# Kernel tuning notes

Hardware: AMD Instinct MI355X
Metric: run time of the kernel (lower is better)

The kernel has to match this reference:

```python
import jax, jax.numpy as jnp
import numpy as np
from jax import lax

NUM_CLASSES = 21
MAX_OUT = 5          # max_output_size in tf.image.non_max_suppression
IOU_THR = 0.5        # NMS_IOU_THRESHOLD
CONF_THR = 0.5       # CONFIDENCE_THRESHOLD
NEG = -1e9           # stand-in for -inf score (suppressed / background)


def setup_inputs() -> dict:
    key = jax.random.key(0)
    k1, k2, k3 = jax.random.split(key, 3)
    B, N, C = 128, 8732, NUM_CLASSES
    logits = jax.random.normal(k1, (B, N, 4 + C), dtype=jnp.float32)
    # default boxes in corner format [ymin, xmin, ymax, xmax], valid geometry
    ctr = jax.random.uniform(k2, (N, 2), dtype=jnp.float32)                 # cy, cx
    sz = jax.random.uniform(k3, (N, 2), dtype=jnp.float32, minval=0.05, maxval=0.3)  # h, w
    default_boxes = jnp.clip(
        jnp.concatenate([ctr - sz / 2, ctr + sz / 2], axis=-1), 0.0, 1.0)
    return {"logits": logits, "default_boxes": default_boxes}


def _decode(loc, db):
    # db: [N,4] corners -> center/size (matches get_offset's tf.stack)
    cy = (db[:, 2] + db[:, 0]) / 2
    cx = (db[:, 3] + db[:, 1]) / 2
    h = db[:, 2] - db[:, 0]
    w = db[:, 3] - db[:, 1]
    # loc: [B,N,4] = (dy, dx, dh, dw)
    ncy = loc[..., 0] * h + cy
    ncx = loc[..., 1] * w + cx
    nh = jnp.exp(loc[..., 2]) * h
    nw = jnp.exp(loc[..., 3]) * w
    boxes = jnp.stack(
        [ncy - nh / 2, ncx - nw / 2, ncy + nh / 2, ncx + nw / 2], axis=-1)
    return jnp.clip(boxes, 0.0, 1.0)


def _iou_one_vs_all(box, boxes):
    # box [4], boxes [N,4], corner format
    tl = jnp.maximum(box[:2], boxes[:, :2])
    br = jnp.minimum(box[2:], boxes[:, 2:])
    wh = jnp.maximum(br - tl, 0.0)
    inter = wh[:, 0] * wh[:, 1]
    a1 = (box[2] - box[0]) * (box[3] - box[1])
    a2 = (boxes[:, 2] - boxes[:, 0]) * (boxes[:, 3] - boxes[:, 1])
    return inter / (a1 + a2 - inter + 1e-12)


def _nms_single(boxes, scores, classes_f):
    # boxes [N,4], scores [N] (background already set to NEG), classes_f [N] float
    def step(s, _):
        i = jnp.argmax(s)
        sc = s[i]
        b = boxes[i]
        valid = sc > CONF_THR  # score_threshold in tf NMS
        iou = _iou_one_vs_all(b, boxes)
        s = jnp.where(iou > IOU_THR, NEG, s)  # suppresses i too (IoU=1)
        return s, (b, classes_f[i], sc, valid)

    _, (bs, cs, ss, vs) = lax.scan(step, scores, None, length=MAX_OUT)
    # pad invalid slots with zeros (TF returns variable-length; we use fixed 5 + zero pad)
    bs = jnp.where(vs[:, None], bs, 0.0)
    cs = jnp.where(vs, cs, 0.0)
    ss = jnp.where(vs, ss, 0.0)
    return bs, cs[:, None], ss[:, None]  # [5,4], [5,1], [5,1]


def reference(logits, default_boxes):
    boxes = _decode(logits[..., :4], default_boxes)          # [B,N,4]
    probs = jax.nn.softmax(logits[..., 4:], axis=-1)         # [B,N,C]
    scores = jnp.max(probs, axis=-1)                          # [B,N]
    classes = jnp.argmax(probs, axis=-1)                      # [B,N] int
    # boolean_mask(classes != 0) expressed as score = -inf for background
    scores_eff = jnp.where(classes != 0, scores, NEG)
    det_b, det_c, det_s = jax.vmap(_nms_single)(
        boxes, scores_eff, classes.astype(jnp.float32))
    # pack detection_boxes / detection_classes / detection_scores -> [B,5,6]
    return jnp.concatenate([det_b, det_c, det_s], axis=-1)
```

## Files before the change

### kernel.cpp

```cpp
#include <hip/hip_runtime.h>

#define NEG (-1e9f)
constexpr int NCLS   = 21;
constexpr int NBOX   = 8732;
constexpr int MAXOUT = 5;
constexpr int CAP    = NBOX;
constexpr float IOU_THR  = 0.5f;
constexpr float CONF_THR = 0.5f;

constexpr int TPB             = 256;
constexpr int BOXES_PER_BLOCK = TPB * 2;
constexpr int BPB             = (NBOX + BOXES_PER_BLOCK - 1) / BOXES_PER_BLOCK;

using u64 = unsigned long long;
typedef float f2_t __attribute__((ext_vector_type(2)));
typedef float f4_t __attribute__((ext_vector_type(4)));


__device__ __forceinline__ u64 pk2(float a, float b) {
    union { float f[2]; u64 u; } x; x.f[0] = a; x.f[1] = b; return x.u;
}
__device__ __forceinline__ float lo2(u64 u) { union { u64 v; float f[2]; } x; x.v = u; return x.f[0]; }
__device__ __forceinline__ float hi2(u64 u) { union { u64 v; float f[2]; } x; x.v = u; return x.f[1]; }

__device__ __forceinline__ void ast(u64* p, u64 v) {
    __hip_atomic_store(p, v, __ATOMIC_RELAXED, __HIP_MEMORY_SCOPE_AGENT);
}
__device__ __forceinline__ u64 ald(const u64* p) {
    return __hip_atomic_load(p, __ATOMIC_RELAXED, __HIP_MEMORY_SCOPE_AGENT);
}

__device__ __forceinline__ void process_box(
        const float* __restrict__ v,
        int b, int n, f4_t db,
        u64* __restrict__ cand,
        int* __restrict__ cnt) {
    float cy = (db[2] + db[0]) * 0.5f;
    float cx = (db[3] + db[1]) * 0.5f;
    float h  = db[2] - db[0];
    float w  = db[3] - db[1];
    float ncy = v[0] * h + cy;
    float ncx = v[1] * w + cx;
    float nh  = expf(v[2]) * h;
    float nw  = expf(v[3]) * w;
    float y1 = fminf(fmaxf(ncy - nh * 0.5f, 0.f), 1.f);
    float x1 = fminf(fmaxf(ncx - nw * 0.5f, 0.f), 1.f);
    float y2 = fminf(fmaxf(ncy + nh * 0.5f, 0.f), 1.f);
    float x2 = fminf(fmaxf(ncx + nw * 0.5f, 0.f), 1.f);

    float m = v[4];
    int am = 0;
#pragma unroll
    for (int j = 1; j < NCLS; j++) {
        float x = v[4 + j];
        if (x > m) { m = x; am = j; }
    }
    float sum = 0.f;
#pragma unroll
    for (int j = 0; j < NCLS; j++) sum += expf(v[4 + j] - m);
    float score = 1.0f / sum;

    if (am != 0 && score > CONF_THR) {
        int p = atomicAdd(&cnt[b], 1);
        if (p < CAP) {
            u64* c = cand + ((long long)b * CAP + p) * 4;
            ast(c + 0, pk2(y1, x1));
            ast(c + 1, pk2(y2, x2));
            ast(c + 2, pk2(score, (float)n));
            ast(c + 3, pk2((float)am, 0.f));
        }
    }
}

__global__ __launch_bounds__(TPB, 8) void fused_kernel(
        const float* __restrict__ logits,
        const float4* __restrict__ dbox4,
        u64* __restrict__ cand,
        int* __restrict__ cnt,
        int* __restrict__ done,
        float* __restrict__ out) {
    const int b   = blockIdx.x / BPB;
    const int blk = blockIdx.x % BPB;
    const int t   = threadIdx.x;
    const int n0  = blk * BOXES_PER_BLOCK + t * 2;

    __shared__ int s_last;

    if (n0 < NBOX) {
        const f2_t* f2  = (const f2_t*)(logits + ((long long)b * NBOX + n0) * 25);
        const f4_t* dbp = (const f4_t*)dbox4;

        float v[25];

        f2_t r[13];
#pragma unroll
        for (int k = 0; k < 13; k++) r[k] = f2[k];
#pragma unroll
        for (int k = 0; k < 12; k++) { v[2 * k] = r[k][0]; v[2 * k + 1] = r[k][1]; }
        v[24] = r[12][0];
        float carry = r[12][1];
        process_box(v, b, n0, dbp[n0], cand, cnt);

        f2_t s[12];
#pragma unroll
        for (int k = 0; k < 12; k++) s[k] = f2[13 + k];
        v[0] = carry;
#pragma unroll
        for (int k = 0; k < 12; k++) { v[1 + 2 * k] = s[k][0]; v[2 + 2 * k] = s[k][1]; }
        process_box(v, b, n0 + 1, dbp[n0 + 1], cand, cnt);
    }

    __syncthreads();
    if (threadIdx.x == 0)
        s_last = (__hip_atomic_fetch_add(&done[b], 1, __ATOMIC_RELAXED,
                                         __HIP_MEMORY_SCOPE_AGENT) == BPB - 1);
    __syncthreads();
    if (!s_last) return;
    if (threadIdx.x >= 64) return;

    const int lane = threadIdx.x;
    const int M = min((int)__hip_atomic_load(&cnt[b], __ATOMIC_RELAXED,
                                             __HIP_MEMORY_SCOPE_AGENT), CAP);
    const u64* cb = cand + (long long)b * CAP * 4;
    float* o = out + (long long)b * MAXOUT * 6;

    int k = 0;
    if (M <= 64) {
        float sc = -INFINITY, oid = 3.0e38f;
        float y1 = 0.f, x1 = 0.f, y2 = 0.f, x2 = 0.f, cls = 0.f;
        if (lane < M) {
            const u64* c = cb + (long long)lane * 4;
            u64 w0 = ald(c + 0), w1 = ald(c + 1), w2 = ald(c + 2), w3 = ald(c + 3);
            y1 = lo2(w0); x1 = hi2(w0);
            y2 = lo2(w1); x2 = hi2(w1);
            sc = lo2(w2); oid = hi2(w2);
            cls = lo2(w3);
        }
        for (; k < MAXOUT; k++) {
            float bv = sc, boid = oid;
            int bi = (lane < M) ? lane : -1;
            for (int mm = 32; mm >= 1; mm >>= 1) {
                float v2 = __shfl_xor(bv,   mm, 64);
                float o2 = __shfl_xor(boid, mm, 64);
                int   i2 = __shfl_xor(bi,   mm, 64);
                if (v2 > bv || (v2 == bv && o2 < boid)) { bv = v2; boid = o2; bi = i2; }
            }
            if (bi < 0 || !(bv > CONF_THR)) break;

            float sy1 = __shfl(y1, bi, 64), sx1 = __shfl(x1, bi, 64);
            float sy2 = __shfl(y2, bi, 64), sx2 = __shfl(x2, bi, 64);
            float scl = __shfl(cls, bi, 64);
            if (lane == 0) {
                o[k * 6 + 0] = sy1; o[k * 6 + 1] = sx1;
                o[k * 6 + 2] = sy2; o[k * 6 + 3] = sx2;
                o[k * 6 + 4] = scl; o[k * 6 + 5] = bv;
            }
            float a1 = (sy2 - sy1) * (sx2 - sx1);
            float tly = fmaxf(sy1, y1);
            float tlx = fmaxf(sx1, x1);
            float bry = fminf(sy2, y2);
            float brx = fminf(sx2, x2);
            float wh0 = fmaxf(bry - tly, 0.f);
            float wh1 = fmaxf(brx - tlx, 0.f);
            float inter = wh0 * wh1;
            float a2 = (y2 - y1) * (x2 - x1);
            float iou = inter / (a1 + a2 - inter + 1e-12f);
            if (lane < M && iou > IOU_THR) sc = NEG;
        }
    } else {
        for (; k < MAXOUT; k++) {
            float bv = -INFINITY, boid = 3.0e38f;
            int bi = -1;
            for (int i = lane; i < M; i += 64) {
                u64 w2 = ald(cb + (long long)i * 4 + 2);
                float v = lo2(w2), od = hi2(w2);
                if (v > bv || (v == bv && od < boid)) { bv = v; boid = od; bi = i; }
            }
            for (int mm = 32; mm >= 1; mm >>= 1) {
                float v2 = __shfl_xor(bv,   mm, 64);
                float o2 = __shfl_xor(boid, mm, 64);
                int   i2 = __shfl_xor(bi,   mm, 64);
                if (v2 > bv || (v2 == bv && o2 < boid)) { bv = v2; boid = o2; bi = i2; }
            }
            if (bi < 0 || !(bv > CONF_THR)) break;

            u64 sw0 = ald(cb + (long long)bi * 4 + 0);
            u64 sw1 = ald(cb + (long long)bi * 4 + 1);
            float sy1 = lo2(sw0), sx1 = hi2(sw0), sy2 = lo2(sw1), sx2 = hi2(sw1);
            if (lane == 0) {
                u64 sw3 = ald(cb + (long long)bi * 4 + 3);
                o[k * 6 + 0] = sy1; o[k * 6 + 1] = sx1;
                o[k * 6 + 2] = sy2; o[k * 6 + 3] = sx2;
                o[k * 6 + 4] = lo2(sw3); o[k * 6 + 5] = bv;
            }
            float a1 = (sy2 - sy1) * (sx2 - sx1);
            for (int i = lane; i < M; i += 64) {
                u64 w0 = ald(cb + (long long)i * 4 + 0);
                u64 w1 = ald(cb + (long long)i * 4 + 1);
                float cy1 = lo2(w0), cx1 = hi2(w0), cy2 = lo2(w1), cx2 = hi2(w1);
                float tly = fmaxf(sy1, cy1);
                float tlx = fmaxf(sx1, cx1);
                float bry = fminf(sy2, cy2);
                float brx = fminf(sx2, cx2);
                float wh0 = fmaxf(bry - tly, 0.f);
                float wh1 = fmaxf(brx - tlx, 0.f);
                float inter = wh0 * wh1;
                float a2 = (cy2 - cy1) * (cx2 - cx1);
                float iou = inter / (a1 + a2 - inter + 1e-12f);
                if (iou > IOU_THR) {
                    u64 w2 = ald(cb + (long long)i * 4 + 2);
                    ast((u64*)(cb + (long long)i * 4 + 2), pk2(NEG, hi2(w2)));
                }
            }
        }
    }
    for (int j = k * 6 + lane; j < MAXOUT * 6; j += 64) o[j] = 0.f;
}

extern "C" void kernel_launch(void* const* d_in, const int* in_sizes, int n_in,
                              void* d_out, int out_size, void* d_ws, size_t ws_size,
                              hipStream_t stream) {
    const float* logits = (const float*)d_in[0];
    const float4* dbox4 = (const float4*)d_in[1];
    float* out          = (float*)d_out;

    const int N = in_sizes[1] / 4;
    const int B = in_sizes[0] / (N * 25);

    int* cnt  = (int*)d_ws;
    int* done = cnt + B;
    u64* cand = (u64*)((char*)d_ws +
        ((2 * (size_t)B * sizeof(int) + 15) & ~(size_t)15));

    hipMemsetAsync(d_ws, 0, 2 * (size_t)B * sizeof(int), stream);
    fused_kernel<<<B * BPB, TPB, 0, stream>>>(logits, dbox4, cand, cnt, done, out);
}
```

Baseline: 187.9 us.

## Process four boxes per thread with float4 loads and a two-pass softmax

Each thread now handles four consecutive boxes, so its 100 floats can be read as 25 aligned float4 loads instead of float2 loads. The max/argmax pass and the exp-sum pass each reread those float4 chunks instead of keeping all values in registers, which trades register pressure for repeated loads served from cache. Box decoding and its exps now run only for boxes that pass the class and confidence filter. The occupancy hint in launch bounds is dropped, and the larger block tile changes how many blocks cover each image.

```diff
diff --git a/kernel.cpp b/kernel.cpp
--- a/kernel.cpp
+++ b/kernel.cpp
@@ -9,11 +9,10 @@
 constexpr float CONF_THR = 0.5f;
 
 constexpr int TPB             = 256;
-constexpr int BOXES_PER_BLOCK = TPB * 2;
+constexpr int BOXES_PER_BLOCK = TPB * 4;
 constexpr int BPB             = (NBOX + BOXES_PER_BLOCK - 1) / BOXES_PER_BLOCK;
 
 using u64 = unsigned long long;
-typedef float f2_t __attribute__((ext_vector_type(2)));
 typedef float f4_t __attribute__((ext_vector_type(4)));
 
 
@@ -30,49 +29,7 @@
     return __hip_atomic_load(p, __ATOMIC_RELAXED, __HIP_MEMORY_SCOPE_AGENT);
 }
 
-__device__ __forceinline__ void process_box(
-        const float* __restrict__ v,
-        int b, int n, f4_t db,
-        u64* __restrict__ cand,
-        int* __restrict__ cnt) {
-    float cy = (db[2] + db[0]) * 0.5f;
-    float cx = (db[3] + db[1]) * 0.5f;
-    float h  = db[2] - db[0];
-    float w  = db[3] - db[1];
-    float ncy = v[0] * h + cy;
-    float ncx = v[1] * w + cx;
-    float nh  = expf(v[2]) * h;
-    float nw  = expf(v[3]) * w;
-    float y1 = fminf(fmaxf(ncy - nh * 0.5f, 0.f), 1.f);
-    float x1 = fminf(fmaxf(ncx - nw * 0.5f, 0.f), 1.f);
-    float y2 = fminf(fmaxf(ncy + nh * 0.5f, 0.f), 1.f);
-    float x2 = fminf(fmaxf(ncx + nw * 0.5f, 0.f), 1.f);
-
-    float m = v[4];
-    int am = 0;
-#pragma unroll
-    for (int j = 1; j < NCLS; j++) {
-        float x = v[4 + j];
-        if (x > m) { m = x; am = j; }
-    }
-    float sum = 0.f;
-#pragma unroll
-    for (int j = 0; j < NCLS; j++) sum += expf(v[4 + j] - m);
-    float score = 1.0f / sum;
-
-    if (am != 0 && score > CONF_THR) {
-        int p = atomicAdd(&cnt[b], 1);
-        if (p < CAP) {
-            u64* c = cand + ((long long)b * CAP + p) * 4;
-            ast(c + 0, pk2(y1, x1));
-            ast(c + 1, pk2(y2, x2));
-            ast(c + 2, pk2(score, (float)n));
-            ast(c + 3, pk2((float)am, 0.f));
-        }
-    }
-}
-
-__global__ __launch_bounds__(TPB, 8) void fused_kernel(
+__global__ __launch_bounds__(TPB) void fused_kernel(
         const float* __restrict__ logits,
         const float4* __restrict__ dbox4,
         u64* __restrict__ cand,
@@ -82,32 +39,85 @@
     const int b   = blockIdx.x / BPB;
     const int blk = blockIdx.x % BPB;
     const int t   = threadIdx.x;
-    const int n0  = blk * BOXES_PER_BLOCK + t * 2;
+    const int n0  = blk * BOXES_PER_BLOCK + t * 4;
 
     __shared__ int s_last;
 
     if (n0 < NBOX) {
-        const f2_t* f2  = (const f2_t*)(logits + ((long long)b * NBOX + n0) * 25);
+        const f4_t* f4  = (const f4_t*)(logits + ((long long)b * NBOX + n0) * 25);
         const f4_t* dbp = (const f4_t*)dbox4;
 
-        float v[25];
-
-        f2_t r[13];
-#pragma unroll
-        for (int k = 0; k < 13; k++) r[k] = f2[k];
-#pragma unroll
-        for (int k = 0; k < 12; k++) { v[2 * k] = r[k][0]; v[2 * k + 1] = r[k][1]; }
-        v[24] = r[12][0];
-        float carry = r[12][1];
-        process_box(v, b, n0, dbp[n0], cand, cnt);
-
-        f2_t s[12];
-#pragma unroll
-        for (int k = 0; k < 12; k++) s[k] = f2[13 + k];
-        v[0] = carry;
-#pragma unroll
-        for (int k = 0; k < 12; k++) { v[1 + 2 * k] = s[k][0]; v[2 + 2 * k] = s[k][1]; }
-        process_box(v, b, n0 + 1, dbp[n0 + 1], cand, cnt);
+        float mx[4];
+        int   am[4];
+        float sm[4];
+        float loc[4][4];
+
+#pragma unroll
+        for (int k = 0; k < 25; k++) {
+            f4_t r = f4[k];
+#pragma unroll
+            for (int c = 0; c < 4; c++) {
+                const int g = 4 * k + c;
+                const int j = g / 25;
+                const int l = g - 25 * j;
+                float x = r[c];
+                if (l < 4) {
+                    loc[j][l] = x;
+                } else if (l == 4) {
+                    mx[j] = x; am[j] = 0;
+                } else {
+                    if (x > mx[j]) { mx[j] = x; am[j] = l - 4; }
+                }
+            }
+        }
+
+        asm volatile("" ::: "memory");
+
+#pragma unroll
+        for (int k = 0; k < 25; k++) {
+            f4_t r = f4[k];
+#pragma unroll
+            for (int c = 0; c < 4; c++) {
+                const int g = 4 * k + c;
+                const int j = g / 25;
+                const int l = g - 25 * j;
+                float x = r[c];
+                if (l == 4) {
+                    sm[j] = expf(x - mx[j]);
+                } else if (l > 4) {
+                    sm[j] += expf(x - mx[j]);
+                }
+            }
+        }
+
+#pragma unroll
+        for (int j = 0; j < 4; j++) {
+            float score = 1.0f / sm[j];
+            if (am[j] != 0 && score > CONF_THR) {
+                f4_t db = dbp[n0 + j];
+                float cy = (db[2] + db[0]) * 0.5f;
+                float cx = (db[3] + db[1]) * 0.5f;
+                float h  = db[2] - db[0];
+                float w  = db[3] - db[1];
+                float ncy = loc[j][0] * h + cy;
+                float ncx = loc[j][1] * w + cx;
+                float nh  = expf(loc[j][2]) * h;
+                float nw  = expf(loc[j][3]) * w;
+                float y1 = fminf(fmaxf(ncy - nh * 0.5f, 0.f), 1.f);
+                float x1 = fminf(fmaxf(ncx - nw * 0.5f, 0.f), 1.f);
+                float y2 = fminf(fmaxf(ncy + nh * 0.5f, 0.f), 1.f);
+                float x2 = fminf(fmaxf(ncx + nw * 0.5f, 0.f), 1.f);
+
+                int p = atomicAdd(&cnt[b], 1);
+                if (p < CAP) {
+                    u64* c = cand + ((long long)b * CAP + p) * 4;
+                    ast(c + 0, pk2(y1, x1));
+                    ast(c + 1, pk2(y2, x2));
+                    ast(c + 2, pk2(score, (float)(n0 + j)));
+                    ast(c + 3, pk2((float)am[j], 0.f));
+                }
+            }
+        }
     }
 
     __syncthreads();
```

Measured after the change: 206.7 us. +10.0%, slower.

## Stage logits tile in LDS with coalesced float4 loads, one box per thread

Applied to the files above, without the earlier changes.

Each block now loads its contiguous slice of logits into shared memory with fully coalesced float4 loads, then each thread reads its 25 floats from LDS and processes a single box. Previously each thread handled two boxes with strided float2 global loads, which coalesce poorly given the 25-float stride. This adds a 25.6KB LDS tile, a barrier, and twice as many blocks, and drops the occupancy hint from launch bounds. The stride-25 LDS reads are odd-strided, so they should be bank-conflict free.

```diff
diff --git a/kernel.cpp b/kernel.cpp
--- a/kernel.cpp
+++ b/kernel.cpp
@@ -9,11 +9,11 @@
 constexpr float CONF_THR = 0.5f;
 
 constexpr int TPB             = 256;
-constexpr int BOXES_PER_BLOCK = TPB * 2;
+constexpr int BOXES_PER_BLOCK = 256;
 constexpr int BPB             = (NBOX + BOXES_PER_BLOCK - 1) / BOXES_PER_BLOCK;
+constexpr int TILE_F4         = BOXES_PER_BLOCK * 25 / 4;
 
 using u64 = unsigned long long;
-typedef float f2_t __attribute__((ext_vector_type(2)));
 typedef float f4_t __attribute__((ext_vector_type(4)));
 
 
@@ -72,7 +72,7 @@
     }
 }
 
-__global__ __launch_bounds__(TPB, 8) void fused_kernel(
+__global__ __launch_bounds__(TPB) void fused_kernel(
         const float* __restrict__ logits,
         const float4* __restrict__ dbox4,
         u64* __restrict__ cand,
@@ -82,32 +82,38 @@
     const int b   = blockIdx.x / BPB;
     const int blk = blockIdx.x % BPB;
     const int t   = threadIdx.x;
-    const int n0  = blk * BOXES_PER_BLOCK + t * 2;
-
+
+    __shared__ __align__(16) f4_t tile4[TILE_F4];
     __shared__ int s_last;
 
-    if (n0 < NBOX) {
-        const f2_t* f2  = (const f2_t*)(logits + ((long long)b * NBOX + n0) * 25);
-        const f4_t* dbp = (const f4_t*)dbox4;
-
+    const int box0 = blk * BOXES_PER_BLOCK;
+    const int nb   = min(BOXES_PER_BLOCK, NBOX - box0);
+    const int nf4  = nb * 25 / 4;
+
+    const f4_t* src = (const f4_t*)(logits + ((long long)b * NBOX + box0) * 25);
+
+    f4_t tmp[7];
+#pragma unroll
+    for (int u = 0; u < 7; u++) {
+        const int i = t + u * TPB;
+        if (i < nf4) tmp[u] = src[i];
+    }
+    f4_t db = {0.f, 0.f, 0.f, 0.f};
+    if (t < nb) db = ((const f4_t*)dbox4)[box0 + t];
+
+#pragma unroll
+    for (int u = 0; u < 7; u++) {
+        const int i = t + u * TPB;
+        if (i < nf4) tile4[i] = tmp[u];
+    }
+    __syncthreads();
+
+    if (t < nb) {
+        const float* tile = (const float*)tile4;
         float v[25];
-
-        f2_t r[13];
-#pragma unroll
-        for (int k = 0; k < 13; k++) r[k] = f2[k];
-#pragma unroll
-        for (int k = 0; k < 12; k++) { v[2 * k] = r[k][0]; v[2 * k + 1] = r[k][1]; }
-        v[24] = r[12][0];
-        float carry = r[12][1];
-        process_box(v, b, n0, dbp[n0], cand, cnt);
-
-        f2_t s[12];
-#pragma unroll
-        for (int k = 0; k < 12; k++) s[k] = f2[13 + k];
-        v[0] = carry;
-#pragma unroll
-        for (int k = 0; k < 12; k++) { v[1 + 2 * k] = s[k][0]; v[2 + 2 * k] = s[k][1]; }
-        process_box(v, b, n0 + 1, dbp[n0 + 1], cand, cnt);
+#pragma unroll
+        for (int k = 0; k < 25; k++) v[k] = tile[t * 25 + k];
+        process_box(v, b, box0 + t, db, cand, cnt);
     }
 
     __syncthreads();
```

New measurement: 215.6 us. 14.7% more time.
